# Kernel optimization log

Measured on AMD Instinct MI355X. Metric: run time of the kernel, lower is better.

## Reference

```python
import jax, jax.numpy as jnp
import numpy as np

H = 768       # hidden_dim
NH = 12       # num_heads
HD = H // NH  # head_dim = 64


def setup_inputs() -> dict:
    key = jax.random.key(0)
    ks = jax.random.split(key, 5)
    scale = 1.0 / np.sqrt(H)
    x = jax.random.normal(ks[0], (16, 1024, H), dtype=jnp.float32)
    W_qkv = jax.random.normal(ks[1], (H, 3 * H), dtype=jnp.float32) * scale
    b_qkv = jnp.zeros((3 * H,), dtype=jnp.float32)
    W_proj = jax.random.normal(ks[2], (H, H), dtype=jnp.float32) * scale
    b_proj = jnp.zeros((H,), dtype=jnp.float32)
    return {"x": x, "W_qkv": W_qkv, "b_qkv": b_qkv, "W_proj": W_proj, "b_proj": b_proj}


def reference(x, W_qkv, b_qkv, W_proj, b_proj):
    bsz, seq_len, hidden = x.shape
    qkv = x @ W_qkv + b_qkv                              # [B,S,3H]
    q, k, v = jnp.split(qkv, 3, axis=-1)
    def heads(t):
        return t.reshape(bsz, seq_len, NH, HD).transpose(0, 2, 1, 3)  # [B,NH,S,HD]
    q, k, v = heads(q), heads(k), heads(v)
    scores = jnp.einsum('bhqd,bhkd->bhqk', q, k) / jnp.sqrt(jnp.float32(HD))
    causal = jnp.tril(jnp.ones((seq_len, seq_len), dtype=bool))
    scores = jnp.where(causal, scores, jnp.finfo(scores.dtype).min)
    attn = jax.nn.softmax(scores, axis=-1)
    out = jnp.einsum('bhqk,bhkd->bhqd', attn, v)         # [B,NH,S,HD]
    out = out.transpose(0, 2, 1, 3).reshape(bsz, seq_len, hidden)
    return out @ W_proj + b_proj
```

## Files before the change

kernel.cpp:

```cpp
#include <hip/hip_runtime.h>

#define H 768
#define NH 12
#define HD 64
#define BSZ 16
#define SEQ 1024
#define MTOK (BSZ * SEQ)
#define N3H (3 * H)

typedef __attribute__((ext_vector_type(8))) short bf16x8;
typedef __attribute__((ext_vector_type(4))) float f32x4;
typedef __attribute__((ext_vector_type(8))) unsigned short us8;
typedef __attribute__((ext_vector_type(4))) unsigned short us4;

__device__ __forceinline__ unsigned short f2bf(float f) {
    union { float f; unsigned u; } v; v.f = f;
    unsigned r = v.u + 0x7fffu + ((v.u >> 16) & 1u);
    return (unsigned short)(r >> 16);
}

typedef __attribute__((address_space(1))) const unsigned int gu32_t;
typedef __attribute__((address_space(3))) unsigned int lu32_t;
__device__ __forceinline__ void glds16(const void* g, void* l) {
    __builtin_amdgcn_global_load_lds((gu32_t*)g, (lu32_t*)l, 16, 0, 0);
}

__global__ __launch_bounds__(256) void cvt_bf16(
    const float* __restrict__ in, unsigned short* __restrict__ out, int n)
{
    int i = (blockIdx.x * 256 + threadIdx.x) * 8;
    if (i >= n) return;
    float4 a = *(const float4*)(in + i);
    float4 b = *(const float4*)(in + i + 4);
    us8 o;
    o[0]=f2bf(a.x); o[1]=f2bf(a.y); o[2]=f2bf(a.z); o[3]=f2bf(a.w);
    o[4]=f2bf(b.x); o[5]=f2bf(b.y); o[6]=f2bf(b.z); o[7]=f2bf(b.w);
    *(us8*)(out + i) = o;
}

__global__ __launch_bounds__(256) void tconv_bf16(
    const float* __restrict__ in, unsigned short* __restrict__ out, int Kd, int Nd)
{
    __shared__ float tile[64][65];
    int t = threadIdx.x;
    int n0 = blockIdx.x * 64, k0 = blockIdx.y * 64;
    #pragma unroll
    for (int r = 0; r < 4; ++r) {
        int kl = r * 16 + (t >> 4);
        float4 v = *(const float4*)(&in[(size_t)(k0 + kl) * Nd + n0 + (t & 15) * 4]);
        tile[kl][(t & 15) * 4 + 0] = v.x; tile[kl][(t & 15) * 4 + 1] = v.y;
        tile[kl][(t & 15) * 4 + 2] = v.z; tile[kl][(t & 15) * 4 + 3] = v.w;
    }
    __syncthreads();
    int nl = t >> 2, kc = (t & 3) * 16;
    us8 o0, o1;
    #pragma unroll
    for (int kk = 0; kk < 8; ++kk) o0[kk] = f2bf(tile[kc + kk][nl]);
    #pragma unroll
    for (int kk = 0; kk < 8; ++kk) o1[kk] = f2bf(tile[kc + 8 + kk][nl]);
    size_t ob = (size_t)(n0 + nl) * Kd + k0 + kc;
    *(us8*)(&out[ob]) = o0;
    *(us8*)(&out[ob + 8]) = o1;
}

__global__ __launch_bounds__(256) void gemm_bf16(
    const unsigned short* __restrict__ A, const unsigned short* __restrict__ BT,
    const float* __restrict__ bias, void* __restrict__ Cout,
    int M, int N, int K, int write_f32)
{
    __shared__ char lds[32768];
    char* As = lds;
    char* Bs = lds + 16384;
    const char* Ac = (const char*)A;
    const char* Bc = (const char*)BT;
    int t = threadIdx.x;
    int l = t & 63, w = t >> 6;
    int l16 = l & 15, l4 = l >> 4;
    int wm = w >> 1, wn = w & 1;
    int rowBase = blockIdx.y * 128, colBase = blockIdx.x * 128;

    f32x4 acc[4][4];
    #pragma unroll
    for (int i = 0; i < 4; ++i)
        #pragma unroll
        for (int j = 0; j < 4; ++j) acc[i][j] = (f32x4){0, 0, 0, 0};

    for (int k0 = 0; k0 < K; k0 += 64) {
        #pragma unroll
        for (int i = 0; i < 4; ++i) {
            int c = t + i * 256;
            int row = c >> 3;
            int src = ((c & 7) * 16) ^ ((row & 7) << 4);
            glds16(Ac + ((size_t)(rowBase + row) * K + k0) * 2 + src, As + c * 16);
            glds16(Bc + ((size_t)(colBase + row) * K + k0) * 2 + src, Bs + c * 16);
        }
        asm volatile("s_waitcnt vmcnt(0)" ::: "memory");
        __builtin_amdgcn_s_barrier();

        #pragma unroll
        for (int kh = 0; kh < 2; ++kh) {
            bf16x8 af[4], bfr[4];
            #pragma unroll
            for (int mi = 0; mi < 4; ++mi) {
                int row = wm * 64 + mi * 16 + l16;
                af[mi] = *(const bf16x8*)(As + row * 128 + ((l4 * 16 + kh * 64) ^ ((row & 7) << 4)));
            }
            #pragma unroll
            for (int ni = 0; ni < 4; ++ni) {
                int row = wn * 64 + ni * 16 + l16;
                bfr[ni] = *(const bf16x8*)(Bs + row * 128 + ((l4 * 16 + kh * 64) ^ ((row & 7) << 4)));
            }
            #pragma unroll
            for (int mi = 0; mi < 4; ++mi)
                #pragma unroll
                for (int ni = 0; ni < 4; ++ni)
                    acc[mi][ni] = __builtin_amdgcn_mfma_f32_16x16x32_bf16(
                        af[mi], bfr[ni], acc[mi][ni], 0, 0, 0);
        }
        __builtin_amdgcn_s_barrier();
    }

    #pragma unroll
    for (int ni = 0; ni < 4; ++ni) {
        int col = colBase + wn * 64 + ni * 16 + l16;
        float bb = bias ? bias[col] : 0.f;
        #pragma unroll
        for (int mi = 0; mi < 4; ++mi) {
            #pragma unroll
            for (int j = 0; j < 4; ++j) {
                int row = rowBase + wm * 64 + mi * 16 + l4 * 4 + j;
                float v = acc[mi][ni][j] + bb;
                if (write_f32) ((float*)Cout)[(size_t)row * N + col] = v;
                else ((unsigned short*)Cout)[(size_t)row * N + col] = f2bf(v);
            }
        }
    }
}

__global__ __launch_bounds__(256) void vtrans(
    const unsigned short* __restrict__ qkvb, unsigned short* __restrict__ vt)
{
    __shared__ char tile[64 * 128];
    int t = threadIdx.x;
    int st = blockIdx.x, h = blockIdx.y, b = blockIdx.z;
    int s0 = st * 64;
    {
        int s = t >> 2, dc = (t & 3) * 16;
        size_t g = (size_t)(b * SEQ + s0 + s) * N3H + 2 * H + h * HD + dc;
        us8 v0 = *(const us8*)(&qkvb[g]);
        us8 v1 = *(const us8*)(&qkvb[g + 8]);
        *(us8*)(tile + s * 128 + ((dc * 2) ^ ((s & 7) << 4))) = v0;
        *(us8*)(tile + s * 128 + ((dc * 2 + 16) ^ ((s & 7) << 4))) = v1;
    }
    __syncthreads();
    int d = t >> 2, sc = (t & 3) * 16;
    us8 o0, o1;
    #pragma unroll
    for (int kk = 0; kk < 8; ++kk) {
        int s = sc + kk;
        o0[kk] = *(const unsigned short*)(tile + s * 128 + ((d * 2) ^ ((s & 7) << 4)));
    }
    #pragma unroll
    for (int kk = 0; kk < 8; ++kk) {
        int s = sc + 8 + kk;
        o1[kk] = *(const unsigned short*)(tile + s * 128 + ((d * 2) ^ ((s & 7) << 4)));
    }
    size_t ob = ((size_t)((b * NH + h) * 64 + d)) * SEQ + s0 + sc;
    *(us8*)(&vt[ob]) = o0;
    *(us8*)(&vt[ob + 8]) = o1;
}

__global__ __launch_bounds__(256) void attn_mfma(
    const unsigned short* __restrict__ qkvb,
    const unsigned short* __restrict__ vt,
    unsigned short* __restrict__ aout)
{
    __shared__ char lds[49152];
    char* Kbuf = lds;
    char* Vbuf = lds + 16384;
    int t = threadIdx.x;
    int l = t & 63, w = t >> 6;
    int l16 = l & 15, l4 = l >> 4;
    int qb = blockIdx.x, h = blockIdx.y, b = blockIdx.z;
    int wqbase = qb * 128 + w * 32;
    int bh = b * NH + h;
    char* Pw = lds + 32768 + w * 4096;
    int nt = 2 * qb + 2;
    int sw = (l16 & 7) << 4;

    const char* qkvc = (const char*)qkvb;
    const char* vtc  = (const char*)vt;

    bf16x8 qB[2][2];
    #pragma unroll
    for (int qs = 0; qs < 2; ++qs) {
        size_t tok = (size_t)(b * SEQ + wqbase + qs * 16 + l16);
        const unsigned short* qrow = qkvb + tok * N3H + h * HD + l4 * 8;
        qB[qs][0] = *(const bf16x8*)(qrow);
        qB[qs][1] = *(const bf16x8*)(qrow + 32);
    }

    auto STAGE = [&](int kt, int bi) {
        #pragma unroll
        for (int i = 0; i < 2; ++i) {
            int c = t + i * 256;
            int row = c >> 3;
            int src = ((c & 7) * 16) ^ ((row & 7) << 4);
            glds16(qkvc + ((size_t)(b * SEQ + kt * 64 + row) * N3H + H + h * HD) * 2 + src,
                   Kbuf + bi * 8192 + c * 16);
        }
        #pragma unroll
        for (int i = 0; i < 2; ++i) {
            int c = t + i * 256;
            int row = c >> 3;
            int src = ((c & 7) * 16) ^ ((row & 7) << 4);
            glds16(vtc + (((size_t)(bh * 64 + row)) * SEQ + kt * 64) * 2 + src,
                   Vbuf + bi * 8192 + c * 16);
        }
    };

    STAGE(0, 0);
    __syncthreads();

    f32x4 o[2][4];
    #pragma unroll
    for (int qs = 0; qs < 2; ++qs)
        #pragma unroll
        for (int dt = 0; dt < 4; ++dt) o[qs][dt] = (f32x4){0, 0, 0, 0};
    float mrun[2] = {-1e30f, -1e30f};
    float lrun[2] = {0.f, 0.f};

    for (int kt = 0; kt < nt; ++kt) {
        int bi = kt & 1;
        if (kt + 1 < nt) {
            STAGE(kt + 1, bi ^ 1);
            asm volatile("s_waitcnt vmcnt(4)" ::: "memory");
        } else {
            asm volatile("s_waitcnt vmcnt(0)" ::: "memory");
        }
        __builtin_amdgcn_s_barrier();

        int ktbase = kt * 64;
        if (ktbase <= wqbase + 31) {
            const char* Kb = Kbuf + bi * 8192;
            const char* Vb = Vbuf + bi * 8192;

            bf16x8 kf[4][2];
            #pragma unroll
            for (int st = 0; st < 4; ++st) {
                int row = st * 16 + l16;
                kf[st][0] = *(const bf16x8*)(Kb + row * 128 + ((l4 * 16) ^ sw));
                kf[st][1] = *(const bf16x8*)(Kb + row * 128 + ((l4 * 16 + 64) ^ sw));
            }

            f32x4 sv[2][4];
            #pragma unroll
            for (int qs = 0; qs < 2; ++qs)
                #pragma unroll
                for (int st = 0; st < 4; ++st) {
                    f32x4 s = (f32x4){0, 0, 0, 0};
                    s = __builtin_amdgcn_mfma_f32_16x16x32_bf16(kf[st][0], qB[qs][0], s, 0, 0, 0);
                    s = __builtin_amdgcn_mfma_f32_16x16x32_bf16(kf[st][1], qB[qs][1], s, 0, 0, 0);
                    sv[qs][st] = s;
                }

            if (ktbase + 63 > wqbase) {
                #pragma unroll
                for (int qs = 0; qs < 2; ++qs) {
                    int q = wqbase + qs * 16 + l16;
                    #pragma unroll
                    for (int st = 0; st < 4; ++st)
                        #pragma unroll
                        for (int r = 0; r < 4; ++r) {
                            int key = ktbase + st * 16 + l4 * 4 + r;
                            if (key > q) sv[qs][st][r] = -3e38f;
                        }
                }
            }

            #pragma unroll
            for (int qs = 0; qs < 2; ++qs) {
                float mx = sv[qs][0][0];
                #pragma unroll
                for (int st = 0; st < 4; ++st)
                    #pragma unroll
                    for (int r = 0; r < 4; ++r) mx = fmaxf(mx, sv[qs][st][r]);
                mx = fmaxf(mx, __shfl_xor(mx, 16, 64));
                mx = fmaxf(mx, __shfl_xor(mx, 32, 64));
                float mnew = fmaxf(mrun[qs], mx * 0.125f);
                float sc = __expf(mrun[qs] - mnew);
                mrun[qs] = mnew;
                float rs = 0.f;
                #pragma unroll
                for (int st = 0; st < 4; ++st)
                    #pragma unroll
                    for (int r = 0; r < 4; ++r) {
                        float p = __expf(fmaf(sv[qs][st][r], 0.125f, -mnew));
                        sv[qs][st][r] = p;
                        rs += p;
                    }
                rs += __shfl_xor(rs, 16, 64);
                rs += __shfl_xor(rs, 32, 64);
                lrun[qs] = lrun[qs] * sc + rs;
                #pragma unroll
                for (int dt = 0; dt < 4; ++dt) {
                    o[qs][dt][0] *= sc; o[qs][dt][1] *= sc;
                    o[qs][dt][2] *= sc; o[qs][dt][3] *= sc;
                }
            }

            #pragma unroll
            for (int qs = 0; qs < 2; ++qs) {
                int row = qs * 16 + l16;
                #pragma unroll
                for (int st = 0; st < 4; ++st) {
                    us4 pk;
                    #pragma unroll
                    for (int r = 0; r < 4; ++r) pk[r] = f2bf(sv[qs][st][r]);
                    *(us4*)(Pw + row * 128 + ((st * 32 + l4 * 8) ^ sw)) = pk;
                }
            }
            bf16x8 pB[2][2];
            #pragma unroll
            for (int qs = 0; qs < 2; ++qs) {
                int row = qs * 16 + l16;
                pB[qs][0] = *(const bf16x8*)(Pw + row * 128 + ((l4 * 16) ^ sw));
                pB[qs][1] = *(const bf16x8*)(Pw + row * 128 + ((l4 * 16 + 64) ^ sw));
            }

            #pragma unroll
            for (int dt = 0; dt < 4; ++dt) {
                int row = dt * 16 + l16;
                bf16x8 v0 = *(const bf16x8*)(Vb + row * 128 + ((l4 * 16) ^ sw));
                bf16x8 v1 = *(const bf16x8*)(Vb + row * 128 + ((l4 * 16 + 64) ^ sw));
                #pragma unroll
                for (int qs = 0; qs < 2; ++qs) {
                    o[qs][dt] = __builtin_amdgcn_mfma_f32_16x16x32_bf16(v0, pB[qs][0], o[qs][dt], 0, 0, 0);
                    o[qs][dt] = __builtin_amdgcn_mfma_f32_16x16x32_bf16(v1, pB[qs][1], o[qs][dt], 0, 0, 0);
                }
            }
        }
        __builtin_amdgcn_s_barrier();
    }

    #pragma unroll
    for (int qs = 0; qs < 2; ++qs) {
        float inv = 1.f / lrun[qs];
        size_t tok = (size_t)(b * SEQ + wqbase + qs * 16 + l16);
        #pragma unroll
        for (int dt = 0; dt < 4; ++dt) {
            us4 ov;
            #pragma unroll
            for (int r = 0; r < 4; ++r) ov[r] = f2bf(o[qs][dt][r] * inv);
            *(us4*)(&aout[tok * H + h * HD + dt * 16 + l4 * 4]) = ov;
        }
    }
}

extern "C" void kernel_launch(void* const* d_in, const int* in_sizes, int n_in,
                              void* d_out, int out_size, void* d_ws, size_t ws_size,
                              hipStream_t stream) {
    const float* x      = (const float*)d_in[0];
    const float* W_qkv  = (const float*)d_in[1];
    const float* b_qkv  = (const float*)d_in[2];
    const float* W_proj = (const float*)d_in[3];
    const float* b_proj = (const float*)d_in[4];
    float* outp = (float*)d_out;

    char* ws = (char*)d_ws;
    unsigned short* xbf    = (unsigned short*)ws;  ws += (size_t)MTOK * H * 2;
    unsigned short* wqkvT  = (unsigned short*)ws;  ws += (size_t)N3H * H * 2;
    unsigned short* wprojT = (unsigned short*)ws;  ws += (size_t)H * H * 2;
    unsigned short* qkvb   = (unsigned short*)ws;  ws += (size_t)MTOK * N3H * 2;
    unsigned short* vtb    = (unsigned short*)ws;  ws += (size_t)BSZ * NH * 64 * SEQ * 2;
    unsigned short* aob    = (unsigned short*)ws;

    cvt_bf16<<<(MTOK * H) / (256 * 8), 256, 0, stream>>>(x, xbf, MTOK * H);
    tconv_bf16<<<dim3(N3H / 64, H / 64), 256, 0, stream>>>(W_qkv, wqkvT, H, N3H);
    tconv_bf16<<<dim3(H / 64, H / 64), 256, 0, stream>>>(W_proj, wprojT, H, H);

    gemm_bf16<<<dim3(N3H / 128, MTOK / 128), 256, 0, stream>>>(
        xbf, wqkvT, b_qkv, qkvb, MTOK, N3H, H, 0);

    vtrans<<<dim3(SEQ / 64, NH, BSZ), 256, 0, stream>>>(qkvb, vtb);

    attn_mfma<<<dim3(SEQ / 128, NH, BSZ), 256, 0, stream>>>(qkvb, vtb, aob);

    gemm_bf16<<<dim3(H / 128, MTOK / 128), 256, 0, stream>>>(
        aob, wprojT, b_proj, (void*)outp, MTOK, H, H, 1);
}
```

Measured before the change: 366.7 us.

## Switch attention to 32x32 MFMA with register P exchange and remap block order

Rewrites the attention inner loop to use 32x32x16 bf16 MFMA tiles, one 32-query tile per wave. The bf16 P matrix is now passed between lanes with cross-lane shuffles instead of a round trip through LDS, which cuts LDS use and allows four blocks per CU. Blocks are remapped to a linear grid that launches the longest causal query blocks first and spreads them across XCD-interleaved chunks, and both GEMMs get a similar XCD-aware block remap. The change also adds s_setprio around the MFMA sections, and it risks higher register pressure under the tighter launch bound.

```diff
diff --git a/kernel.cpp b/kernel.cpp
--- a/kernel.cpp
+++ b/kernel.cpp
@@ -10,6 +10,7 @@
 
 typedef __attribute__((ext_vector_type(8))) short bf16x8;
 typedef __attribute__((ext_vector_type(4))) float f32x4;
+typedef __attribute__((ext_vector_type(16))) float f32x16;
 typedef __attribute__((ext_vector_type(8))) unsigned short us8;
 typedef __attribute__((ext_vector_type(4))) unsigned short us4;
 
@@ -77,7 +78,12 @@
     int l = t & 63, w = t >> 6;
     int l16 = l & 15, l4 = l >> 4;
     int wm = w >> 1, wn = w & 1;
-    int rowBase = blockIdx.y * 128, colBase = blockIdx.x * 128;
+
+    int chunk = (int)gridDim.x >> 3;
+    int lin = (blockIdx.x & 7) * chunk + (blockIdx.x >> 3);
+    int nbx = N >> 7;
+    int bx = lin % nbx, by = lin / nbx;
+    int rowBase = by * 128, colBase = bx * 128;
 
     f32x4 acc[4][4];
     #pragma unroll
@@ -170,34 +176,36 @@
     *(us8*)(&vt[ob + 8]) = o1;
 }
 
-__global__ __launch_bounds__(256) void attn_mfma(
+__global__ __launch_bounds__(256, 4) void attn_mfma(
     const unsigned short* __restrict__ qkvb,
     const unsigned short* __restrict__ vt,
     unsigned short* __restrict__ aout)
 {
-    __shared__ char lds[49152];
+    __shared__ char lds[32768];
     char* Kbuf = lds;
     char* Vbuf = lds + 16384;
     int t = threadIdx.x;
     int l = t & 63, w = t >> 6;
-    int l16 = l & 15, l4 = l >> 4;
-    int qb = blockIdx.x, h = blockIdx.y, b = blockIdx.z;
-    int wqbase = qb * 128 + w * 32;
-    int bh = b * NH + h;
-    char* Pw = lds + 32768 + w * 4096;
+    int l31 = l & 31, b5 = l >> 5;
+
+    int lin = ((blockIdx.x & 7) * 192) + (blockIdx.x >> 3);
+    int qb = 7 - (lin & 7);
+    int bh = lin >> 3;
+    int h = bh % NH, b = bh / NH;
+
+    int wq = qb * 128 + w * 32;
+    int sw31 = (l31 & 7) << 4;
     int nt = 2 * qb + 2;
-    int sw = (l16 & 7) << 4;
-
+    int bhh = b * NH + h;
     const char* qkvc = (const char*)qkvb;
     const char* vtc  = (const char*)vt;
 
-    bf16x8 qB[2][2];
-    #pragma unroll
-    for (int qs = 0; qs < 2; ++qs) {
-        size_t tok = (size_t)(b * SEQ + wqbase + qs * 16 + l16);
-        const unsigned short* qrow = qkvb + tok * N3H + h * HD + l4 * 8;
-        qB[qs][0] = *(const bf16x8*)(qrow);
-        qB[qs][1] = *(const bf16x8*)(qrow + 32);
+    bf16x8 qB[4];
+    {
+        const unsigned short* qrow =
+            qkvb + (size_t)(b * SEQ + wq + l31) * N3H + h * HD + b5 * 8;
+        #pragma unroll
+        for (int m = 0; m < 4; ++m) qB[m] = *(const bf16x8*)(qrow + m * 16);
     }
 
     auto STAGE = [&](int kt, int bi) {
@@ -214,7 +222,7 @@
             int c = t + i * 256;
             int row = c >> 3;
             int src = ((c & 7) * 16) ^ ((row & 7) << 4);
-            glds16(vtc + (((size_t)(bh * 64 + row)) * SEQ + kt * 64) * 2 + src,
+            glds16(vtc + (((size_t)(bhh * 64 + row)) * SEQ + kt * 64) * 2 + src,
                    Vbuf + bi * 8192 + c * 16);
         }
     };
@@ -222,13 +230,10 @@
     STAGE(0, 0);
     __syncthreads();
 
-    f32x4 o[2][4];
-    #pragma unroll
-    for (int qs = 0; qs < 2; ++qs)
-        #pragma unroll
-        for (int dt = 0; dt < 4; ++dt) o[qs][dt] = (f32x4){0, 0, 0, 0};
-    float mrun[2] = {-1e30f, -1e30f};
-    float lrun[2] = {0.f, 0.f};
+    f32x16 o0, o1;
+    #pragma unroll
+    for (int r = 0; r < 16; ++r) { o0[r] = 0.f; o1[r] = 0.f; }
+    float mrun = -1e30f, lrun = 0.f;
 
     for (int kt = 0; kt < nt; ++kt) {
         int bi = kt & 1;
@@ -241,119 +246,107 @@
         __builtin_amdgcn_s_barrier();
 
         int ktbase = kt * 64;
-        if (ktbase <= wqbase + 31) {
+        if (ktbase <= wq + 31) {
             const char* Kb = Kbuf + bi * 8192;
             const char* Vb = Vbuf + bi * 8192;
 
-            bf16x8 kf[4][2];
-            #pragma unroll
-            for (int st = 0; st < 4; ++st) {
-                int row = st * 16 + l16;
-                kf[st][0] = *(const bf16x8*)(Kb + row * 128 + ((l4 * 16) ^ sw));
-                kf[st][1] = *(const bf16x8*)(Kb + row * 128 + ((l4 * 16 + 64) ^ sw));
-            }
-
-            f32x4 sv[2][4];
-            #pragma unroll
-            for (int qs = 0; qs < 2; ++qs)
-                #pragma unroll
-                for (int st = 0; st < 4; ++st) {
-                    f32x4 s = (f32x4){0, 0, 0, 0};
-                    s = __builtin_amdgcn_mfma_f32_16x16x32_bf16(kf[st][0], qB[qs][0], s, 0, 0, 0);
-                    s = __builtin_amdgcn_mfma_f32_16x16x32_bf16(kf[st][1], qB[qs][1], s, 0, 0, 0);
-                    sv[qs][st] = s;
+            f32x16 s[2];
+            __builtin_amdgcn_s_setprio(1);
+            #pragma unroll
+            for (int st2 = 0; st2 < 2; ++st2) {
+                f32x16 acc;
+                #pragma unroll
+                for (int r = 0; r < 16; ++r) acc[r] = 0.f;
+                #pragma unroll
+                for (int m = 0; m < 4; ++m) {
+                    int row = st2 * 32 + l31;
+                    bf16x8 kf = *(const bf16x8*)(Kb + row * 128 + ((m * 32 + b5 * 16) ^ sw31));
+                    acc = __builtin_amdgcn_mfma_f32_32x32x16_bf16(kf, qB[m], acc, 0, 0, 0);
                 }
-
-            if (ktbase + 63 > wqbase) {
-                #pragma unroll
-                for (int qs = 0; qs < 2; ++qs) {
-                    int q = wqbase + qs * 16 + l16;
+                s[st2] = acc;
+            }
+            __builtin_amdgcn_s_setprio(0);
+
+            if (ktbase + 63 > wq) {
+                int q = wq + l31;
+                #pragma unroll
+                for (int st2 = 0; st2 < 2; ++st2)
                     #pragma unroll
-                    for (int st = 0; st < 4; ++st)
-                        #pragma unroll
-                        for (int r = 0; r < 4; ++r) {
-                            int key = ktbase + st * 16 + l4 * 4 + r;
-                            if (key > q) sv[qs][st][r] = -3e38f;
-                        }
+                    for (int r = 0; r < 16; ++r) {
+                        int key = ktbase + st2 * 32 + (r & 3) + 8 * (r >> 2) + 4 * b5;
+                        if (key > q) s[st2][r] = -3e38f;
+                    }
+            }
+
+            float mx = s[0][0];
+            #pragma unroll
+            for (int r = 1; r < 16; ++r) mx = fmaxf(mx, s[0][r]);
+            #pragma unroll
+            for (int r = 0; r < 16; ++r) mx = fmaxf(mx, s[1][r]);
+            mx = fmaxf(mx, __shfl_xor(mx, 32, 64));
+            float mnew = fmaxf(mrun, mx * 0.125f);
+            float sc = __expf(mrun - mnew);
+            mrun = mnew;
+            float rs = 0.f;
+            #pragma unroll
+            for (int st2 = 0; st2 < 2; ++st2)
+                #pragma unroll
+                for (int r = 0; r < 16; ++r) {
+                    float p = __expf(fmaf(s[st2][r], 0.125f, -mnew));
+                    s[st2][r] = p;
+                    rs += p;
                 }
-            }
-
-            #pragma unroll
-            for (int qs = 0; qs < 2; ++qs) {
-                float mx = sv[qs][0][0];
-                #pragma unroll
-                for (int st = 0; st < 4; ++st)
-                    #pragma unroll
-                    for (int r = 0; r < 4; ++r) mx = fmaxf(mx, sv[qs][st][r]);
-                mx = fmaxf(mx, __shfl_xor(mx, 16, 64));
-                mx = fmaxf(mx, __shfl_xor(mx, 32, 64));
-                float mnew = fmaxf(mrun[qs], mx * 0.125f);
-                float sc = __expf(mrun[qs] - mnew);
-                mrun[qs] = mnew;
-                float rs = 0.f;
-                #pragma unroll
-                for (int st = 0; st < 4; ++st)
-                    #pragma unroll
-                    for (int r = 0; r < 4; ++r) {
-                        float p = __expf(fmaf(sv[qs][st][r], 0.125f, -mnew));
-                        sv[qs][st][r] = p;
-                        rs += p;
-                    }
-                rs += __shfl_xor(rs, 16, 64);
-                rs += __shfl_xor(rs, 32, 64);
-                lrun[qs] = lrun[qs] * sc + rs;
-                #pragma unroll
-                for (int dt = 0; dt < 4; ++dt) {
-                    o[qs][dt][0] *= sc; o[qs][dt][1] *= sc;
-                    o[qs][dt][2] *= sc; o[qs][dt][3] *= sc;
-                }
-            }
-
-            #pragma unroll
-            for (int qs = 0; qs < 2; ++qs) {
-                int row = qs * 16 + l16;
-                #pragma unroll
-                for (int st = 0; st < 4; ++st) {
-                    us4 pk;
-                    #pragma unroll
-                    for (int r = 0; r < 4; ++r) pk[r] = f2bf(sv[qs][st][r]);
-                    *(us4*)(Pw + row * 128 + ((st * 32 + l4 * 8) ^ sw)) = pk;
-                }
-            }
-            bf16x8 pB[2][2];
-            #pragma unroll
-            for (int qs = 0; qs < 2; ++qs) {
-                int row = qs * 16 + l16;
-                pB[qs][0] = *(const bf16x8*)(Pw + row * 128 + ((l4 * 16) ^ sw));
-                pB[qs][1] = *(const bf16x8*)(Pw + row * 128 + ((l4 * 16 + 64) ^ sw));
-            }
-
-            #pragma unroll
-            for (int dt = 0; dt < 4; ++dt) {
-                int row = dt * 16 + l16;
-                bf16x8 v0 = *(const bf16x8*)(Vb + row * 128 + ((l4 * 16) ^ sw));
-                bf16x8 v1 = *(const bf16x8*)(Vb + row * 128 + ((l4 * 16 + 64) ^ sw));
-                #pragma unroll
-                for (int qs = 0; qs < 2; ++qs) {
-                    o[qs][dt] = __builtin_amdgcn_mfma_f32_16x16x32_bf16(v0, pB[qs][0], o[qs][dt], 0, 0, 0);
-                    o[qs][dt] = __builtin_amdgcn_mfma_f32_16x16x32_bf16(v1, pB[qs][1], o[qs][dt], 0, 0, 0);
-                }
-            }
+            rs += __shfl_xor(rs, 32, 64);
+            lrun = lrun * sc + rs;
+            #pragma unroll
+            for (int r = 0; r < 16; ++r) { o0[r] *= sc; o1[r] *= sc; }
+
+            bf16x8 pB[4];
+            #pragma unroll
+            for (int wd = 0; wd < 4; ++wd) {
+                int st2 = wd >> 1, hf = (wd & 1) * 8;
+                unsigned pk0 = (unsigned)f2bf(s[st2][hf + 0]) | ((unsigned)f2bf(s[st2][hf + 1]) << 16);
+                unsigned pk1 = (unsigned)f2bf(s[st2][hf + 2]) | ((unsigned)f2bf(s[st2][hf + 3]) << 16);
+                unsigned pk2 = (unsigned)f2bf(s[st2][hf + 4]) | ((unsigned)f2bf(s[st2][hf + 5]) << 16);
+                unsigned pk3 = (unsigned)f2bf(s[st2][hf + 6]) | ((unsigned)f2bf(s[st2][hf + 7]) << 16);
+                unsigned snd0 = b5 ? pk0 : pk2;
+                unsigned snd1 = b5 ? pk1 : pk3;
+                unsigned r0 = (unsigned)__shfl_xor((int)snd0, 32, 64);
+                unsigned r1 = (unsigned)__shfl_xor((int)snd1, 32, 64);
+                union { unsigned u[4]; bf16x8 v; } cvt;
+                cvt.u[0] = b5 ? r0 : pk0;
+                cvt.u[1] = b5 ? r1 : pk1;
+                cvt.u[2] = b5 ? pk2 : r0;
+                cvt.u[3] = b5 ? pk3 : r1;
+                pB[wd] = cvt.v;
+            }
+
+            __builtin_amdgcn_s_setprio(1);
+            #pragma unroll
+            for (int wd = 0; wd < 4; ++wd) {
+                bf16x8 v0 = *(const bf16x8*)(Vb + l31 * 128 + ((wd * 32 + b5 * 16) ^ sw31));
+                o0 = __builtin_amdgcn_mfma_f32_32x32x16_bf16(v0, pB[wd], o0, 0, 0, 0);
+                bf16x8 v1 = *(const bf16x8*)(Vb + (32 + l31) * 128 + ((wd * 32 + b5 * 16) ^ sw31));
+                o1 = __builtin_amdgcn_mfma_f32_32x32x16_bf16(v1, pB[wd], o1, 0, 0, 0);
+            }
+            __builtin_amdgcn_s_setprio(0);
         }
         __builtin_amdgcn_s_barrier();
     }
 
-    #pragma unroll
-    for (int qs = 0; qs < 2; ++qs) {
-        float inv = 1.f / lrun[qs];
-        size_t tok = (size_t)(b * SEQ + wqbase + qs * 16 + l16);
-        #pragma unroll
-        for (int dt = 0; dt < 4; ++dt) {
-            us4 ov;
-            #pragma unroll
-            for (int r = 0; r < 4; ++r) ov[r] = f2bf(o[qs][dt][r] * inv);
-            *(us4*)(&aout[tok * H + h * HD + dt * 16 + l4 * 4]) = ov;
-        }
+    float inv = 1.f / lrun;
+    size_t tok = (size_t)(b * SEQ + wq + l31);
+    #pragma unroll
+    for (int g = 0; g < 4; ++g) {
+        us4 w0, w1;
+        #pragma unroll
+        for (int j = 0; j < 4; ++j) {
+            w0[j] = f2bf(o0[g * 4 + j] * inv);
+            w1[j] = f2bf(o1[g * 4 + j] * inv);
+        }
+        int d0 = g * 8 + b5 * 4;
+        *(us4*)(&aout[tok * H + h * HD + d0]) = w0;
+        *(us4*)(&aout[tok * H + h * HD + 32 + d0]) = w1;
     }
 }
 
@@ -379,13 +372,13 @@
     tconv_bf16<<<dim3(N3H / 64, H / 64), 256, 0, stream>>>(W_qkv, wqkvT, H, N3H);
     tconv_bf16<<<dim3(H / 64, H / 64), 256, 0, stream>>>(W_proj, wprojT, H, H);
 
-    gemm_bf16<<<dim3(N3H / 128, MTOK / 128), 256, 0, stream>>>(
+    gemm_bf16<<<(N3H / 128) * (MTOK / 128), 256, 0, stream>>>(
         xbf, wqkvT, b_qkv, qkvb, MTOK, N3H, H, 0);
 
     vtrans<<<dim3(SEQ / 64, NH, BSZ), 256, 0, stream>>>(qkvb, vtb);
 
-    attn_mfma<<<dim3(SEQ / 128, NH, BSZ), 256, 0, stream>>>(qkvb, vtb, aob);
-
-    gemm_bf16<<<dim3(H / 128, MTOK / 128), 256, 0, stream>>>(
+    attn_mfma<<<(SEQ / 128) * NH * BSZ, 256, 0, stream>>>(qkvb, vtb, aob);
+
+    gemm_bf16<<<(H / 128) * (MTOK / 128), 256, 0, stream>>>(
         aob, wprojT, b_proj, (void*)outp, MTOK, H, H, 1);
 }
```

After: 317.8 us. 13.3% less time.
